# Kernel tuning notes

Hardware: AMD Instinct MI355X
Metric: run time of the kernel (lower is better)

Reference implementation:

```python
import jax, jax.numpy as jnp
from jax import lax
import numpy as np

B, T = 64, 50
N_POINTS, N_STATE, N_ACTION = 3, 6, 2
ROWS = COLS = 64          # local env window
RES = 0.03                # meters / pixel
PADDING = 200
H_FULL = W_FULL = 256
FC = 256
C_IN = N_POINTS + 1 + N_ACTION  # rope channels + local env + action smear
FLAT = 32 * 14 * 14


def setup_inputs() -> dict:
    key = jax.random.key(0)
    ks = jax.random.split(key, 10)
    action = jax.random.normal(ks[0], (B, T, N_ACTION), jnp.float32) * 0.1
    state = jax.random.normal(ks[1], (B, T + 1, N_STATE), jnp.float32) * 0.3
    res = jnp.full((B, T, 1), RES, jnp.float32)
    full_env = (jax.random.uniform(ks[2], (B, H_FULL, W_FULL)) > 0.9).astype(jnp.float32)
    full_env_origin = jnp.full((B, 2), H_FULL / 2, jnp.float32)
    conv_w1 = jax.random.normal(ks[3], (3, 3, C_IN, 16), jnp.float32) * 0.1
    conv_b1 = jnp.zeros((16,), jnp.float32)
    conv_w2 = jax.random.normal(ks[4], (3, 3, 16, 32), jnp.float32) * 0.1
    conv_b2 = jnp.zeros((32,), jnp.float32)
    d_in = N_STATE + N_ACTION + FLAT
    dense_w0 = jax.random.normal(ks[5], (d_in, FC), jnp.float32) * 0.01
    dense_b0 = jnp.zeros((FC,), jnp.float32)
    dense_w1 = jax.random.normal(ks[6], (FC, FC), jnp.float32) * 0.01
    dense_b1 = jnp.zeros((FC,), jnp.float32)
    dense_w2 = jax.random.normal(ks[7], (FC, N_STATE), jnp.float32) * 0.01
    dense_b2 = jnp.zeros((N_STATE,), jnp.float32)
    return dict(action=action, state=state, res=res, full_env=full_env,
                full_env_origin=full_env_origin,
                conv_w1=conv_w1, conv_b1=conv_b1, conv_w2=conv_w2, conv_b2=conv_b2,
                dense_w0=dense_w0, dense_b0=dense_b0, dense_w1=dense_w1,
                dense_b1=dense_b1, dense_w2=dense_w2, dense_b2=dense_b2)


def _forward(action, state, res, full_env, full_env_origin,
             conv_w1, conv_b1, conv_w2, conv_b2,
             dense_w0, dense_b0, dense_w1, dense_b1, dense_w2, dense_b2):
    s0 = state[:, 0]                     # [B, N_STATE]
    res0 = res[:, 0, 0]                  # [B]
    origin = full_env_origin             # [B, 2] (row, col) pixel origin
    padded = jnp.pad(full_env, ((0, 0), (PADDING, PADDING), (PADDING, PADDING)))
    bi = jnp.arange(B)
    dr = jnp.arange(-(ROWS // 2), ROWS // 2)
    dc = jnp.arange(-(COLS // 2), COLS // 2)
    half = jnp.array([ROWS // 2, COLS // 2], jnp.float32)
    pi = jnp.arange(N_POINTS)[None, :]

    def raster(points, local_origin):
        # points [B, P, 2] (x, y) meters; local_origin [B, 2] (row, col)
        r = (points[..., 1] / res0[:, None] + local_origin[:, 0:1]).astype(jnp.int32)
        c = (points[..., 0] / res0[:, None] + local_origin[:, 1:2]).astype(jnp.int32)
        valid = (r >= 0) & (r < ROWS) & (c >= 0) & (c < COLS)
        rc = jnp.clip(r, 0, ROWS - 1)
        cc = jnp.clip(c, 0, COLS - 1)
        img = jnp.zeros((B, ROWS, COLS, N_POINTS), jnp.float32)
        img = img.at[bi[:, None], rc, cc, pi].add(valid.astype(jnp.float32))
        return jnp.minimum(img, 1.0)

    def step(s_t, a_t):
        head = s_t[:, -2:]                                   # (x, y) of head point
        ccol = (head[:, 0] / RES + origin[:, 1]).astype(jnp.int32)
        crow = (head[:, 1] / RES + origin[:, 0]).astype(jnp.int32)
        ri = crow[:, None, None] + dr[None, :, None] + PADDING   # [B, ROWS, COLS]
        ci = ccol[:, None, None] + dc[None, None, :] + PADDING
        local = padded[bi[:, None, None], ri, ci]                # gather local window
        local_origin = origin - jnp.stack([crow, ccol], 1).astype(jnp.float32) + half
        rope_img = raster(s_t.reshape(B, N_POINTS, 2), local_origin)
        act_img = jnp.broadcast_to(a_t[:, None, None, :], (B, ROWS, COLS, N_ACTION))
        z = jnp.concatenate([rope_img, local[..., None], act_img], axis=-1)
        for w, b in ((conv_w1, conv_b1), (conv_w2, conv_b2)):
            z = jax.nn.relu(lax.conv_general_dilated(
                z, w, (1, 1), 'VALID',
                dimension_numbers=('NHWC', 'HWIO', 'NHWC')) + b)
            z = lax.reduce_window(z, -jnp.inf, lax.max,
                                  (1, 2, 2, 1), (1, 2, 2, 1), 'VALID')
        z = z.reshape(B, -1)
        h = jnp.concatenate([s_t, a_t, z], axis=-1)              # mixed
        h = jax.nn.relu(h @ dense_w0 + dense_b0)
        h = jax.nn.relu(h @ dense_w1 + dense_b1)
        ds = h @ dense_w2 + dense_b2
        s_next = s_t + ds                                        # residual
        return s_next, s_next

    _, traj = lax.scan(step, s0, jnp.swapaxes(action, 0, 1))     # traj [T, B, N_STATE]
    return jnp.concatenate([s0[:, None], jnp.swapaxes(traj, 0, 1)], axis=1)


def reference(action, state, res, full_env, full_env_origin,
              conv_w1, conv_b1, conv_w2, conv_b2,
              dense_w0, dense_b0, dense_w1, dense_b1, dense_w2, dense_b2):
    return _forward(action, state, res, full_env, full_env_origin,
                    conv_w1, conv_b1, conv_w2, conv_b2,
                    dense_w0, dense_b0, dense_w1, dense_b1, dense_w2, dense_b2)
```

## Files before the change

### kernel.cpp

```cpp
#include <hip/hip_runtime.h>


__global__ __launch_bounds__(256, 2)
void k_tc(const float* __restrict__ action, const float* __restrict__ state,
          const float* __restrict__ res, const float* __restrict__ env,
          const float* __restrict__ origin,
          const float* __restrict__ w1, const float* __restrict__ b1,
          const float* __restrict__ w2, const float* __restrict__ b2,
          const float* __restrict__ w0, const float* __restrict__ b0,
          const float* __restrict__ w1d, const float* __restrict__ b1d,
          const float* __restrict__ w2d, const float* __restrict__ b2d,
          const float* __restrict__ wsPart, float* __restrict__ wsS,
          float* __restrict__ wsFlatT, float* __restrict__ out, int st)
{
    const int wg  = blockIdx.x;
    const int b   = wg >> 3;
    const int oct = wg & 7;
    const int tid = threadIdx.x;

    __shared__ float w1l[864];
    __shared__ float w2l[4608];
    __shared__ float b2l[32];
    __shared__ float bAl[16];
    __shared__ float sSl[8];
    __shared__ int   prm[12];
    __shared__ float h1l[256];
    __shared__ float wred[24];
    __shared__ float pool1s[6*31*20];
    __shared__ unsigned char inl[14*64];

    if (st < 50){
        for (int i = tid; i < 216; i += 256)
            *(float4*)&w1l[i*4] = *(const float4*)(w1 + i*4);
        for (int i = tid; i < 1152; i += 256)
            *(float4*)&w2l[i*4] = *(const float4*)(w2 + i*4);
        if (tid < 32) b2l[tid] = b2[tid];
    }

    if (st == 0){
        if (tid < 6) sSl[tid] = state[b*306 + tid];
        __syncthreads();
    } else {
        const float* sp = wsS + ((st-1)&1)*512 + b*8;
        const float a0p = action[b*100 + (st-1)*2 + 0];
        const float a1p = action[b*100 + (st-1)*2 + 1];
        const int col = tid;

        float hacc = b0[col];
        #pragma unroll
        for (int j = 0; j < 6; j++) hacc = fmaf(sp[j], w0[j*256 + col], hacc);
        hacc = fmaf(a0p, w0[1536 + col], hacc);
        hacc = fmaf(a1p, w0[1792 + col], hacc);
        {
            const float* pp = wsPart + b*8192 + col;
            float e0 = 0.f, e1 = 0.f;
            #pragma unroll
            for (int ks = 0; ks < 32; ks += 2){
                e0 += pp[ks*256];
                e1 += pp[(ks+1)*256];
            }
            hacc += e0 + e1;
        }
        h1l[col] = fmaxf(hacc, 0.f);
        __syncthreads();

        float d0 = b1d[col], d1 = 0.f;
        const float* wc = w1d + col;
        #pragma unroll 8
        for (int k = 0; k < 256; k += 2){
            d0 = fmaf(h1l[k],   wc[k*256],     d0);
            d1 = fmaf(h1l[k+1], wc[(k+1)*256], d1);
        }
        float h2 = fmaxf(d0 + d1, 0.f);

        float p[6];
        const float* wr = w2d + col*6;
        #pragma unroll
        for (int j = 0; j < 6; j++) p[j] = h2 * wr[j];
        #pragma unroll
        for (int off = 32; off > 0; off >>= 1){
            #pragma unroll
            for (int j = 0; j < 6; j++) p[j] += __shfl_down(p[j], off, 64);
        }
        if ((tid & 63) == 0){
            #pragma unroll
            for (int j = 0; j < 6; j++) wred[(tid >> 6)*6 + j] = p[j];
        }
        __syncthreads();
        if (tid < 6){
            float ds = wred[tid] + wred[6+tid] + wred[12+tid] + wred[18+tid] + b2d[tid];
            sSl[tid] = sp[tid] + ds;
        }
        __syncthreads();
    }

    if (oct == 0 && tid < 6){
        out[b*306 + st*6 + tid] = sSl[tid];
        wsS[(st & 1)*512 + b*8 + tid] = sSl[tid];
    }
    if (st >= 50) return;

    if (tid == 0){
        float org0 = origin[2*b], org1 = origin[2*b+1];
        int ccol = (int)(sSl[4] / 0.03f + org1);
        int crow = (int)(sSl[5] / 0.03f + org0);
        float res0 = res[b*50];
        float lo0 = org0 - (float)crow + 32.0f;
        float lo1 = org1 - (float)ccol + 32.0f;
        prm[0] = crow; prm[1] = ccol;
        #pragma unroll
        for (int p = 0; p < 3; p++){
            int rr = (int)(sSl[2*p+1]/res0 + lo0);
            int cc = (int)(sSl[2*p  ]/res0 + lo1);
            prm[2+p] = rr; prm[5+p] = cc;
            prm[8+p] = (rr>=0 && rr<64 && cc>=0 && cc<64) ? 1 : 0;
        }
    }
    if (tid < 16){
        float s4 = 0.f, s5 = 0.f;
        #pragma unroll
        for (int k = 0; k < 9; k++){
            s4 += w1[(k*6 + 4)*16 + tid];
            s5 += w1[(k*6 + 5)*16 + tid];
        }
        float a0 = action[b*100 + st*2 + 0];
        float a1 = action[b*100 + st*2 + 1];
        bAl[tid] = b1[tid] + a0*s4 + a1*s5;
    }
    __syncthreads();

    const int p2lo = (oct < 6) ? 2*oct : 12 + (oct - 6);
    const int p2n  = (oct < 6) ? 2 : 1;
    const int p1n  = 2*p2n + 2;
    const int p1lo = 2*p2lo;
    const int ilo  = 4*p2lo;
    const int inn  = 2*p1n + 2;

    {
        const int crow = prm[0], ccol = prm[1];
        for (int idx = tid; idx < inn*64; idx += 256){
            int i = idx >> 6, j = idx & 63;
            int r = crow - 32 + ilo + i;
            int c = ccol - 32 + j;
            float v = (r>=0 && r<256 && c>=0 && c<256) ? env[b*65536 + (r<<8) + c] : 0.f;
            inl[idx] = (unsigned char)v;
        }
    }
    __syncthreads();

    {
        int pr[3], pc[3], pvld[3];
        #pragma unroll
        for (int p = 0; p < 3; p++){ pr[p]=prm[2+p]; pc[p]=prm[5+p]; pvld[p]=prm[8+p]; }

        for (int u = tid; u < p1n*31; u += 256){
            int pl = u / 31;
            int j  = u - pl*31;
            float l[4][4];
            #pragma unroll
            for (int dy = 0; dy < 4; dy++)
                #pragma unroll
                for (int dx = 0; dx < 4; dx++)
                    l[dy][dx] = (float)inl[(2*pl + dy)*64 + 2*j + dx];

            float m[16];
            #pragma unroll
            for (int o = 0; o < 16; o++) m[o] = 0.f;

            #pragma unroll
            for (int dy = 0; dy < 2; dy++){
                #pragma unroll
                for (int dx = 0; dx < 2; dx++){
                    int rg = 2*(p1lo + pl) + dy;
                    int cg = 2*j + dx;
                    bool pf[3]; int pidx[3];
                    #pragma unroll
                    for (int p = 0; p < 3; p++){
                        int kr = pr[p] - rg, kc = pc[p] - cg;
                        pf[p] = pvld[p] && kr >= 0 && kr < 3 && kc >= 0 && kc < 3;
                        pidx[p] = pf[p] ? ((kr*3 + kc)*6 + p)*16 : 0;
                    }
                    #pragma unroll
                    for (int o = 0; o < 16; o++){
                        float v = bAl[o];
                        #pragma unroll
                        for (int kr = 0; kr < 3; kr++)
                            #pragma unroll
                            for (int kc = 0; kc < 3; kc++)
                                v = fmaf(l[dy+kr][dx+kc], w1l[((kr*3 + kc)*6 + 3)*16 + o], v);
                        if (pf[0]) v += w1l[pidx[0] + o];
                        if (pf[1]) v += w1l[pidx[1] + o];
                        if (pf[2]) v += w1l[pidx[2] + o];
                        v = fmaxf(v, 0.f);
                        m[o] = fmaxf(m[o], v);
                    }
                }
            }
            float* pd = &pool1s[(pl*31 + j)*20];
            *(float4*)(pd     ) = make_float4(m[0],  m[1],  m[2],  m[3]);
            *(float4*)(pd + 4 ) = make_float4(m[4],  m[5],  m[6],  m[7]);
            *(float4*)(pd + 8 ) = make_float4(m[8],  m[9],  m[10], m[11]);
            *(float4*)(pd + 12) = make_float4(m[12], m[13], m[14], m[15]);
        }
    }
    __syncthreads();

    for (int u = tid; u < p2n*14*8; u += 256){
        int pi  = u / 112;
        int rem = u - pi*112;
        int jj  = rem >> 3;
        int oq  = rem & 7;
        int o0  = oq*4;

        float acc[4][4];
        #pragma unroll
        for (int ps = 0; ps < 4; ps++)
            #pragma unroll
            for (int c = 0; c < 4; c++) acc[ps][c] = 0.f;

        #pragma unroll 1
        for (int t9 = 0; t9 < 9; t9++){
            int kr = t9 / 3, kc = t9 - 3*(t9/3);
            const float* pb = &pool1s[((2*pi + kr)*31 + (2*jj + kc))*20];
            const float* wb = &w2l[(kr*3 + kc)*512 + o0];
            #pragma unroll
            for (int kib = 0; kib < 4; kib++){
                float4 q00 = *(const float4*)(pb + kib*4);
                float4 q01 = *(const float4*)(pb + 20 + kib*4);
                float4 q10 = *(const float4*)(pb + 620 + kib*4);
                float4 q11 = *(const float4*)(pb + 640 + kib*4);
                float pq[4][4] = {
                    {q00.x, q00.y, q00.z, q00.w},
                    {q01.x, q01.y, q01.z, q01.w},
                    {q10.x, q10.y, q10.z, q10.w},
                    {q11.x, q11.y, q11.z, q11.w}};
                #pragma unroll
                for (int kk = 0; kk < 4; kk++){
                    float4 wv = *(const float4*)(wb + (kib*4 + kk)*32);
                    #pragma unroll
                    for (int ps = 0; ps < 4; ps++){
                        float pvv = pq[ps][kk];
                        acc[ps][0] = fmaf(pvv, wv.x, acc[ps][0]);
                        acc[ps][1] = fmaf(pvv, wv.y, acc[ps][1]);
                        acc[ps][2] = fmaf(pvv, wv.z, acc[ps][2]);
                        acc[ps][3] = fmaf(pvv, wv.w, acc[ps][3]);
                    }
                }
            }
        }
        int kb = ((p2lo + pi)*14 + jj)*32 + o0;
        #pragma unroll
        for (int c = 0; c < 4; c++){
            float bb = b2l[o0 + c];
            float v0 = fmaxf(acc[0][c] + bb, 0.f);
            float v1 = fmaxf(acc[1][c] + bb, 0.f);
            float v2 = fmaxf(acc[2][c] + bb, 0.f);
            float v3 = fmaxf(acc[3][c] + bb, 0.f);
            wsFlatT[(kb + c)*64 + b] = fmaxf(fmaxf(v0, v1), fmaxf(v2, v3));
        }
    }
}

__global__ __launch_bounds__(256, 2)
void k_dense0(const float* __restrict__ w0, const float* __restrict__ wsFlatT,
              float* __restrict__ wsPart)
{
    const int blk = blockIdx.x;
    const int lid = (blk & 7)*64 + (blk >> 3);
    const int ks = lid >> 4;
    const int nc = lid & 15;
    const int n0 = nc*16;
    const int tid  = threadIdx.x;
    const int w    = tid >> 6;
    const int lane = tid & 63;
    const int mg = lane >> 2;
    const int nq = lane & 3;
    const int kbase = ks*196;

    __shared__ float xs[196*68];

    for (int idx = tid; idx < 3136; idx += 256){
        int k  = idx >> 4;
        int b4 = idx & 15;
        float4 v = *(const float4*)(wsFlatT + (kbase + k)*64 + b4*4);
        *(float4*)(&xs[k*68 + b4*4]) = v;
    }
    __syncthreads();

    float acc[4][4];
    #pragma unroll
    for (int i = 0; i < 4; i++)
        #pragma unroll
        for (int c = 0; c < 4; c++) acc[i][c] = 0.f;

    const float* xk = xs + (49*w)*68 + mg*4;
    const float* wpp = w0 + (8 + kbase + 49*w)*256 + n0 + nq*4;
    #pragma unroll 7
    for (int k = 0; k < 49; k++){
        float4 x4 = *(const float4*)(xk + k*68);
        float4 w4 = *(const float4*)(wpp + k*256);
        acc[0][0]=fmaf(x4.x,w4.x,acc[0][0]); acc[0][1]=fmaf(x4.x,w4.y,acc[0][1]);
        acc[0][2]=fmaf(x4.x,w4.z,acc[0][2]); acc[0][3]=fmaf(x4.x,w4.w,acc[0][3]);
        acc[1][0]=fmaf(x4.y,w4.x,acc[1][0]); acc[1][1]=fmaf(x4.y,w4.y,acc[1][1]);
        acc[1][2]=fmaf(x4.y,w4.z,acc[1][2]); acc[1][3]=fmaf(x4.y,w4.w,acc[1][3]);
        acc[2][0]=fmaf(x4.z,w4.x,acc[2][0]); acc[2][1]=fmaf(x4.z,w4.y,acc[2][1]);
        acc[2][2]=fmaf(x4.z,w4.z,acc[2][2]); acc[2][3]=fmaf(x4.z,w4.w,acc[2][3]);
        acc[3][0]=fmaf(x4.w,w4.x,acc[3][0]); acc[3][1]=fmaf(x4.w,w4.y,acc[3][1]);
        acc[3][2]=fmaf(x4.w,w4.z,acc[3][2]); acc[3][3]=fmaf(x4.w,w4.w,acc[3][3]);
    }
    __syncthreads();

    float* red = xs;
    {
        float* rr = red + (w*64 + lane)*17;
        #pragma unroll
        for (int j = 0; j < 16; j++) rr[j] = acc[j>>2][j&3];
    }
    __syncthreads();
    if (tid < 64){
        int mg2 = tid >> 2, nq2 = tid & 3;
        #pragma unroll
        for (int g = 0; g < 4; g++){
            float4 v;
            v.x = red[tid*17+4*g+0] + red[(64+tid)*17+4*g+0] + red[(128+tid)*17+4*g+0] + red[(192+tid)*17+4*g+0];
            v.y = red[tid*17+4*g+1] + red[(64+tid)*17+4*g+1] + red[(128+tid)*17+4*g+1] + red[(192+tid)*17+4*g+1];
            v.z = red[tid*17+4*g+2] + red[(64+tid)*17+4*g+2] + red[(128+tid)*17+4*g+2] + red[(192+tid)*17+4*g+2];
            v.w = red[tid*17+4*g+3] + red[(64+tid)*17+4*g+3] + red[(128+tid)*17+4*g+3] + red[(192+tid)*17+4*g+3];
            int bb = mg2*4 + g;
            *(float4*)(wsPart + (bb*32 + ks)*256 + n0 + nq2*4) = v;
        }
    }
}

extern "C" void kernel_launch(void* const* d_in, const int* in_sizes, int n_in,
                              void* d_out, int out_size, void* d_ws, size_t ws_size,
                              hipStream_t stream)
{
    (void)in_sizes; (void)n_in; (void)out_size; (void)ws_size;
    const float* action = (const float*)d_in[0];
    const float* state  = (const float*)d_in[1];
    const float* res    = (const float*)d_in[2];
    const float* env    = (const float*)d_in[3];
    const float* origin = (const float*)d_in[4];
    const float* w1  = (const float*)d_in[5];
    const float* b1  = (const float*)d_in[6];
    const float* w2  = (const float*)d_in[7];
    const float* b2  = (const float*)d_in[8];
    const float* w0  = (const float*)d_in[9];
    const float* b0  = (const float*)d_in[10];
    const float* w1d = (const float*)d_in[11];
    const float* b1d = (const float*)d_in[12];
    const float* w2d = (const float*)d_in[13];
    const float* b2d = (const float*)d_in[14];
    float* out = (float*)d_out;

    float* wsF     = (float*)d_ws;
    float* wsS     = wsF;
    float* wsFlatT = wsF + 1024;
    float* wsPart  = wsF + 1024 + 401408;

    for (int st = 0; st <= 50; ++st){
        k_tc<<<dim3(512), dim3(256), 0, stream>>>(
            action, state, res, env, origin, w1, b1, w2, b2, w0, b0,
            w1d, b1d, w2d, b2d, wsPart, wsS, wsFlatT, out, st);
        if (st < 50)
            k_dense0<<<dim3(512), dim3(256), 0, stream>>>(w0, wsFlatT, wsPart);
    }
}
```

Before: 2.036 ms.

## Split redundant dense tail out of conv kernel into a parallel tail kernel

```diff
diff --git a/kernel.cpp b/kernel.cpp
--- a/kernel.cpp
+++ b/kernel.cpp
@@ -1,17 +1,107 @@
 #include <hip/hip_runtime.h>
 
 
+__global__ __launch_bounds__(512)
+void k_tail(const float* __restrict__ action, const float* __restrict__ w0,
+            const float* __restrict__ b0, const float* __restrict__ w1d,
+            const float* __restrict__ wsPart, const float* __restrict__ wsS,
+            float* __restrict__ wsD1p, int st)
+{
+    const int b   = blockIdx.x >> 2;
+    const int q   = blockIdx.x & 3;
+    const int tid = threadIdx.x;
+
+    __shared__ float hp[512];
+    __shared__ float h1l[64];
+    __shared__ float dp[512];
+
+    const float* sp = wsS + ((st-1)&1)*512 + b*8;
+    const float a0p = action[b*100 + (st-1)*2 + 0];
+    const float a1p = action[b*100 + (st-1)*2 + 1];
+
+    {
+        const int cl  = tid & 63;
+        const int ksg = tid >> 6;
+        const int col = q*64 + cl;
+        const float* pp = wsPart + b*8192 + ksg*4*256 + col;
+        float h = pp[0] + pp[256] + pp[512] + pp[768];
+        if (ksg == 0){
+            h += b0[col];
+            #pragma unroll
+            for (int j = 0; j < 6; j++) h = fmaf(sp[j], w0[j*256 + col], h);
+            h = fmaf(a0p, w0[1536 + col], h);
+            h = fmaf(a1p, w0[1792 + col], h);
+        }
+        hp[tid] = h;
+    }
+    __syncthreads();
+    if (tid < 64){
+        float s = hp[tid]       + hp[64 + tid]  + hp[128 + tid] + hp[192 + tid]
+                + hp[256 + tid] + hp[320 + tid] + hp[384 + tid] + hp[448 + tid];
+        h1l[tid] = fmaxf(s, 0.f);
+    }
+    __syncthreads();
+
+    {
+        const int colp = tid & 255;
+        const int kh   = tid >> 8;
+        const float* wrow = w1d + (q*64 + kh*32)*256 + colp;
+        const float* hh   = h1l + kh*32;
+        float d0 = 0.f, d1 = 0.f;
+        #pragma unroll 8
+        for (int k = 0; k < 32; k += 2){
+            d0 = fmaf(hh[k],   wrow[k*256],     d0);
+            d1 = fmaf(hh[k+1], wrow[(k+1)*256], d1);
+        }
+        dp[tid] = d0 + d1;
+    }
+    __syncthreads();
+    if (tid < 256)
+        wsD1p[b*1024 + q*256 + tid] = dp[tid] + dp[256 + tid];
+}
+
+__device__ inline void tail_finish(int b, int tid, int st,
+                                   const float* __restrict__ wsD1p,
+                                   const float* __restrict__ b1d,
+                                   const float* __restrict__ w2d,
+                                   const float* __restrict__ b2d,
+                                   const float* __restrict__ wsS,
+                                   float* __restrict__ wred,
+                                   float* __restrict__ sSl)
+{
+    const float* dd = wsD1p + b*1024 + tid;
+    float h2 = fmaxf(dd[0] + dd[256] + dd[512] + dd[768] + b1d[tid], 0.f);
+    float p[6];
+    const float* wr = w2d + tid*6;
+    #pragma unroll
+    for (int j = 0; j < 6; j++) p[j] = h2 * wr[j];
+    #pragma unroll
+    for (int off = 32; off > 0; off >>= 1){
+        #pragma unroll
+        for (int j = 0; j < 6; j++) p[j] += __shfl_down(p[j], off, 64);
+    }
+    if ((tid & 63) == 0){
+        #pragma unroll
+        for (int j = 0; j < 6; j++) wred[(tid >> 6)*6 + j] = p[j];
+    }
+    __syncthreads();
+    if (tid < 6){
+        float ds = wred[tid] + wred[6+tid] + wred[12+tid] + wred[18+tid] + b2d[tid];
+        sSl[tid] = wsS[((st-1)&1)*512 + b*8 + tid] + ds;
+    }
+    __syncthreads();
+}
+
 __global__ __launch_bounds__(256, 2)
-void k_tc(const float* __restrict__ action, const float* __restrict__ state,
-          const float* __restrict__ res, const float* __restrict__ env,
-          const float* __restrict__ origin,
-          const float* __restrict__ w1, const float* __restrict__ b1,
-          const float* __restrict__ w2, const float* __restrict__ b2,
-          const float* __restrict__ w0, const float* __restrict__ b0,
-          const float* __restrict__ w1d, const float* __restrict__ b1d,
-          const float* __restrict__ w2d, const float* __restrict__ b2d,
-          const float* __restrict__ wsPart, float* __restrict__ wsS,
-          float* __restrict__ wsFlatT, float* __restrict__ out, int st)
+void k_conv(const float* __restrict__ action, const float* __restrict__ state,
+            const float* __restrict__ res, const float* __restrict__ env,
+            const float* __restrict__ origin,
+            const float* __restrict__ w1, const float* __restrict__ b1,
+            const float* __restrict__ w2, const float* __restrict__ b2,
+            const float* __restrict__ b1d, const float* __restrict__ w2d,
+            const float* __restrict__ b2d, const float* __restrict__ wsD1p,
+            float* __restrict__ wsS, float* __restrict__ wsFlatT,
+            float* __restrict__ out, int st)
 {
     const int wg  = blockIdx.x;
     const int b   = wg >> 3;
@@ -23,82 +113,28 @@
     __shared__ float b2l[32];
     __shared__ float bAl[16];
     __shared__ float sSl[8];
+    __shared__ float wred[24];
     __shared__ int   prm[12];
-    __shared__ float h1l[256];
-    __shared__ float wred[24];
     __shared__ float pool1s[6*31*20];
     __shared__ unsigned char inl[14*64];
 
-    if (st < 50){
-        for (int i = tid; i < 216; i += 256)
-            *(float4*)&w1l[i*4] = *(const float4*)(w1 + i*4);
-        for (int i = tid; i < 1152; i += 256)
-            *(float4*)&w2l[i*4] = *(const float4*)(w2 + i*4);
-        if (tid < 32) b2l[tid] = b2[tid];
-    }
+    for (int i = tid; i < 216; i += 256)
+        *(float4*)&w1l[i*4] = *(const float4*)(w1 + i*4);
+    for (int i = tid; i < 1152; i += 256)
+        *(float4*)&w2l[i*4] = *(const float4*)(w2 + i*4);
+    if (tid < 32) b2l[tid] = b2[tid];
 
     if (st == 0){
         if (tid < 6) sSl[tid] = state[b*306 + tid];
         __syncthreads();
     } else {
-        const float* sp = wsS + ((st-1)&1)*512 + b*8;
-        const float a0p = action[b*100 + (st-1)*2 + 0];
-        const float a1p = action[b*100 + (st-1)*2 + 1];
-        const int col = tid;
-
-        float hacc = b0[col];
-        #pragma unroll
-        for (int j = 0; j < 6; j++) hacc = fmaf(sp[j], w0[j*256 + col], hacc);
-        hacc = fmaf(a0p, w0[1536 + col], hacc);
-        hacc = fmaf(a1p, w0[1792 + col], hacc);
-        {
-            const float* pp = wsPart + b*8192 + col;
-            float e0 = 0.f, e1 = 0.f;
-            #pragma unroll
-            for (int ks = 0; ks < 32; ks += 2){
-                e0 += pp[ks*256];
-                e1 += pp[(ks+1)*256];
-            }
-            hacc += e0 + e1;
-        }
-        h1l[col] = fmaxf(hacc, 0.f);
-        __syncthreads();
-
-        float d0 = b1d[col], d1 = 0.f;
-        const float* wc = w1d + col;
-        #pragma unroll 8
-        for (int k = 0; k < 256; k += 2){
-            d0 = fmaf(h1l[k],   wc[k*256],     d0);
-            d1 = fmaf(h1l[k+1], wc[(k+1)*256], d1);
-        }
-        float h2 = fmaxf(d0 + d1, 0.f);
-
-        float p[6];
-        const float* wr = w2d + col*6;
-        #pragma unroll
-        for (int j = 0; j < 6; j++) p[j] = h2 * wr[j];
-        #pragma unroll
-        for (int off = 32; off > 0; off >>= 1){
-            #pragma unroll
-            for (int j = 0; j < 6; j++) p[j] += __shfl_down(p[j], off, 64);
-        }
-        if ((tid & 63) == 0){
-            #pragma unroll
-            for (int j = 0; j < 6; j++) wred[(tid >> 6)*6 + j] = p[j];
-        }
-        __syncthreads();
-        if (tid < 6){
-            float ds = wred[tid] + wred[6+tid] + wred[12+tid] + wred[18+tid] + b2d[tid];
-            sSl[tid] = sp[tid] + ds;
-        }
-        __syncthreads();
+        tail_finish(b, tid, st, wsD1p, b1d, w2d, b2d, wsS, wred, sSl);
     }
 
     if (oct == 0 && tid < 6){
         out[b*306 + st*6 + tid] = sSl[tid];
         wsS[(st & 1)*512 + b*8 + tid] = sSl[tid];
     }
-    if (st >= 50) return;
 
     if (tid == 0){
         float org0 = origin[2*b], org1 = origin[2*b+1];
@@ -332,6 +368,19 @@
     }
 }
 
+__global__ __launch_bounds__(256)
+void k_fin(const float* __restrict__ b1d, const float* __restrict__ w2d,
+           const float* __restrict__ b2d, const float* __restrict__ wsD1p,
+           const float* __restrict__ wsS, float* __restrict__ out)
+{
+    const int b = blockIdx.x;
+    const int tid = threadIdx.x;
+    __shared__ float wred[24];
+    __shared__ float sSl[8];
+    tail_finish(b, tid, 50, wsD1p, b1d, w2d, b2d, wsS, wred, sSl);
+    if (tid < 6) out[b*306 + 300 + tid] = sSl[tid];
+}
+
 extern "C" void kernel_launch(void* const* d_in, const int* in_sizes, int n_in,
                               void* d_out, int out_size, void* d_ws, size_t ws_size,
                               hipStream_t stream)
@@ -356,14 +405,24 @@
 
     float* wsF     = (float*)d_ws;
     float* wsS     = wsF;
-    float* wsFlatT = wsF + 1024;
-    float* wsPart  = wsF + 1024 + 401408;
-
-    for (int st = 0; st <= 50; ++st){
-        k_tc<<<dim3(512), dim3(256), 0, stream>>>(
-            action, state, res, env, origin, w1, b1, w2, b2, w0, b0,
-            w1d, b1d, w2d, b2d, wsPart, wsS, wsFlatT, out, st);
-        if (st < 50)
-            k_dense0<<<dim3(512), dim3(256), 0, stream>>>(w0, wsFlatT, wsPart);
-    }
-}
+    float* wsD1p   = wsF + 1024;
+    float* wsFlatT = wsF + 1024 + 65536;
+    float* wsPart  = wsF + 1024 + 65536 + 401408;
+
+    k_conv<<<dim3(512), dim3(256), 0, stream>>>(
+        action, state, res, env, origin, w1, b1, w2, b2,
+        b1d, w2d, b2d, wsD1p, wsS, wsFlatT, out, 0);
+    k_dense0<<<dim3(512), dim3(256), 0, stream>>>(w0, wsFlatT, wsPart);
+
+    for (int st = 1; st < 50; ++st){
+        k_tail<<<dim3(256), dim3(512), 0, stream>>>(
+            action, w0, b0, w1d, wsPart, wsS, wsD1p, st);
+        k_conv<<<dim3(512), dim3(256), 0, stream>>>(
+            action, state, res, env, origin, w1, b1, w2, b2,
+            b1d, w2d, b2d, wsD1p, wsS, wsFlatT, out, st);
+        k_dense0<<<dim3(512), dim3(256), 0, stream>>>(w0, wsFlatT, wsPart);
+    }
+    k_tail<<<dim3(256), dim3(512), 0, stream>>>(
+        action, w0, b0, w1d, wsPart, wsS, wsD1p, 50);
+    k_fin<<<dim3(64), dim3(256), 0, stream>>>(b1d, w2d, b2d, wsD1p, wsS, out);
+}
```

Result: faster. 1.811 ms (-11.0%).
